# Performance work log

Hardware: AMD Instinct MI355X
Metric: run time of the kernel (lower is better)

## Reference

```python
import jax, jax.numpy as jnp
import numpy as np

B, S, D = 4, 1024, 1024
H, DK, DV = 16, 64, 32
SCALE = float(np.sqrt(DK))


def setup_inputs() -> dict:
    key = jax.random.key(0)
    ks = jax.random.split(key, 10)
    std = 0.02
    x = jax.random.normal(ks[0], (B, S, D), dtype=jnp.float32)
    # Per-head projection weights stacked: y = x @ W + b (equiv to torch Linear)
    Wq = jax.random.normal(ks[1], (H, D, DK), dtype=jnp.float32) * std
    bq = jax.random.normal(ks[2], (H, DK), dtype=jnp.float32) * std
    Wk = jax.random.normal(ks[3], (H, D, DK), dtype=jnp.float32) * std
    bk = jax.random.normal(ks[4], (H, DK), dtype=jnp.float32) * std
    Wv = jax.random.normal(ks[5], (H, D, DV), dtype=jnp.float32) * std
    bv = jax.random.normal(ks[6], (H, DV), dtype=jnp.float32) * std
    Wo = jax.random.normal(ks[7], (H * DV, D), dtype=jnp.float32) * std
    bo = jax.random.normal(ks[8], (D,), dtype=jnp.float32) * std
    return {"x": x, "Wq": Wq, "bq": bq, "Wk": Wk, "bk": bk,
            "Wv": Wv, "bv": bv, "Wo": Wo, "bo": bo}


def reference(x, Wq, bq, Wk, bk, Wv, bv, Wo, bo):
    # batched per-head projections (vectorizes the torch per-head loop)
    q = jnp.einsum('bsd,hdk->bhsk', x, Wq) + bq[None, :, None, :]
    k = jnp.einsum('bsd,hdk->bhsk', x, Wk) + bk[None, :, None, :]
    v = jnp.einsum('bsd,hdv->bhsv', x, Wv) + bv[None, :, None, :]
    # scaled dot-product attention (no mask path)
    scores = jnp.einsum('bhsk,bhtk->bhst', q, k) / SCALE  # [B,H,S,S]
    weights = jax.nn.softmax(scores, axis=-1)
    out_h = jnp.einsum('bhst,bhtv->bhsv', weights, v)      # [B,H,S,DV]
    # concat heads in head order (matches torch.cat over head_outputs)
    concat = out_h.transpose(0, 2, 1, 3).reshape(B, S, H * DV)
    output = concat @ Wo + bo  # dropout p=0 / eval -> identity
    return (output, weights)
```

## Files before the change

### kernel.cpp

```cpp
#include <hip/hip_runtime.h>
#include <cstdint>
#include <cstddef>

#define BB 4
#define SS 1024
#define DD 1024
#define HH 16
#define DKK 64
#define DVV 32
#define LOG2E 1.44269504088896340736f

typedef __bf16 bf16_t;
typedef __bf16 bf16x8 __attribute__((ext_vector_type(8)));
typedef float f32x4 __attribute__((ext_vector_type(4)));

__device__ inline bf16x8 cvt8(const float* __restrict__ s) {
  float4 a = *(const float4*)s;
  float4 b = *(const float4*)(s + 4);
  bf16x8 r;
  r[0] = (__bf16)a.x; r[1] = (__bf16)a.y; r[2] = (__bf16)a.z; r[3] = (__bf16)a.w;
  r[4] = (__bf16)b.x; r[5] = (__bf16)b.y; r[6] = (__bf16)b.z; r[7] = (__bf16)b.w;
  return r;
}

__global__ __launch_bounds__(256) void transpose_cvt_kernel(
    const float* __restrict__ src, bf16_t* __restrict__ dst,
    int M, int N, size_t srcStride, size_t dstStride) {
  __shared__ __align__(16) bf16_t T[64][72];
  const int tid = threadIdx.x;
  const int n0 = blockIdx.x * 64, m0 = blockIdx.y * 64;
  const float* s = src + (size_t)blockIdx.z * srcStride;
  bf16_t* d = dst + (size_t)blockIdx.z * dstStride;
  const int rr = tid >> 3, c8 = (tid & 7) * 8;

  if (n0 + c8 < N) {
#pragma unroll
    for (int mm = rr; mm < 64; mm += 32) {
      const float* p = s + (size_t)(m0 + mm) * N + n0 + c8;
      float4 a = *(const float4*)p;
      float4 b = *(const float4*)(p + 4);
      T[c8 + 0][mm] = (__bf16)a.x; T[c8 + 1][mm] = (__bf16)a.y;
      T[c8 + 2][mm] = (__bf16)a.z; T[c8 + 3][mm] = (__bf16)a.w;
      T[c8 + 4][mm] = (__bf16)b.x; T[c8 + 5][mm] = (__bf16)b.y;
      T[c8 + 6][mm] = (__bf16)b.z; T[c8 + 7][mm] = (__bf16)b.w;
    }
  }
  __syncthreads();
#pragma unroll
  for (int rn = rr; rn < 64; rn += 32) {
    if (n0 + rn < N)
      *(uint4*)(d + (size_t)(n0 + rn) * M + m0 + c8) = *(uint4*)&T[rn][c8];
  }
}

__global__ __launch_bounds__(256) void qkv_gemm_kernel(
    const float* __restrict__ X, const bf16_t* __restrict__ WT,
    const float* __restrict__ bq, const float* __restrict__ bk,
    const float* __restrict__ bv,
    bf16_t* __restrict__ Qw, bf16_t* __restrict__ Kw, bf16_t* __restrict__ VT) {
  __shared__ __align__(16) bf16_t As[64][72];
  __shared__ __align__(16) bf16_t Bs[64][72];
  const int m0 = blockIdx.x * 64;
  const int n0 = blockIdx.y * 64;
  const int tid = threadIdx.x;
  const int wave = tid >> 6;
  const int lane = tid & 63;
  const int g = lane >> 4;
  const int ln = lane & 15;
  const int r = tid >> 3;
  const int c8 = (tid & 7) * 8;

  f32x4 acc[4] = {};

  for (int k0 = 0; k0 < 1024; k0 += 64) {
    *(bf16x8*)&As[r][c8]      = cvt8(X + (size_t)(m0 + r) * 1024 + k0 + c8);
    *(bf16x8*)&As[r + 32][c8] = cvt8(X + (size_t)(m0 + r + 32) * 1024 + k0 + c8);
    *(uint4*)&Bs[r][c8]      = *(const uint4*)(WT + (size_t)(n0 + r) * 1024 + k0 + c8);
    *(uint4*)&Bs[r + 32][c8] = *(const uint4*)(WT + (size_t)(n0 + r + 32) * 1024 + k0 + c8);
    __syncthreads();
#pragma unroll
    for (int ks = 0; ks < 2; ks++) {
      bf16x8 a = *(const bf16x8*)&As[wave * 16 + ln][ks * 32 + g * 8];
#pragma unroll
      for (int ns = 0; ns < 4; ns++) {
        bf16x8 b = *(const bf16x8*)&Bs[ns * 16 + ln][ks * 32 + g * 8];
        acc[ns] = __builtin_amdgcn_mfma_f32_16x16x32_bf16(a, b, acc[ns], 0, 0, 0);
      }
    }
    __syncthreads();
  }

#pragma unroll
  for (int ns = 0; ns < 4; ns++) {
    int c = n0 + ns * 16 + ln;
    float bias = (c < 1024) ? bq[c] : (c < 2048 ? bk[c - 1024] : bv[c - 2048]);
#pragma unroll
    for (int i = 0; i < 4; i++) {
      int m = m0 + wave * 16 + g * 4 + i;
      float v = acc[ns][i] + bias;
      int b_ = m >> 10, s_ = m & 1023;
      if (c < 1024) {
        int h = c >> 6, k = c & 63;
        Qw[(((size_t)(b_ * HH + h)) * SS + s_) * DKK + k] = (__bf16)(v * 0.125f);
      } else if (c < 2048) {
        int c2 = c - 1024;
        int h = c2 >> 6, k = c2 & 63;
        Kw[(((size_t)(b_ * HH + h)) * SS + s_) * DKK + k] = (__bf16)v;
      } else {
        int c2 = c - 2048;
        int h = c2 >> 5, vv = c2 & 31;
        VT[(((size_t)(b_ * HH + h)) * DVV + vv) * SS + s_] = (__bf16)v;
      }
    }
  }
}

__global__ __launch_bounds__(256) void attn_softmax_kernel(
    const bf16_t* __restrict__ Qw, const bf16_t* __restrict__ Kw,
    float* __restrict__ Wout) {
  __shared__ __align__(16) bf16_t Qs[64][72];
  __shared__ __align__(16) bf16_t Ks[64][72];
  const int bh = blockIdx.y;
  const int m0 = blockIdx.x * 64;
  const int tid = threadIdx.x;
  const int wave = tid >> 6;
  const int lane = tid & 63;
  const int g = lane >> 4;
  const int ln = lane & 15;
  const int r = tid >> 3;
  const int c8 = (tid & 7) * 8;

  const bf16_t* Qbase = Qw + (size_t)bh * SS * DKK;
  const bf16_t* Kbase = Kw + (size_t)bh * SS * DKK;

  *(uint4*)&Qs[r][c8]      = *(const uint4*)(Qbase + (size_t)(m0 + r) * DKK + c8);
  *(uint4*)&Qs[r + 32][c8] = *(const uint4*)(Qbase + (size_t)(m0 + r + 32) * DKK + c8);
  __syncthreads();

  float mrun[4] = {-1e30f, -1e30f, -1e30f, -1e30f};
  float lrun[4] = {0.f, 0.f, 0.f, 0.f};

  for (int jt = 0; jt < 16; jt++) {
    *(uint4*)&Ks[r][c8]      = *(const uint4*)(Kbase + (size_t)(jt * 64 + r) * DKK + c8);
    *(uint4*)&Ks[r + 32][c8] = *(const uint4*)(Kbase + (size_t)(jt * 64 + r + 32) * DKK + c8);
    __syncthreads();
    f32x4 acc[4] = {};
#pragma unroll
    for (int ks = 0; ks < 2; ks++) {
      bf16x8 a = *(const bf16x8*)&Qs[wave * 16 + ln][ks * 32 + g * 8];
#pragma unroll
      for (int ns = 0; ns < 4; ns++) {
        bf16x8 b = *(const bf16x8*)&Ks[ns * 16 + ln][ks * 32 + g * 8];
        acc[ns] = __builtin_amdgcn_mfma_f32_16x16x32_bf16(a, b, acc[ns], 0, 0, 0);
      }
    }
#pragma unroll
    for (int ns = 0; ns < 4; ns++) {
#pragma unroll
      for (int i = 0; i < 4; i++) {
        float p = acc[ns][i] * LOG2E;
        float mo = mrun[i];
        float mn = fmaxf(mo, p);
        lrun[i] = lrun[i] * exp2f(mo - mn) + exp2f(p - mn);
        mrun[i] = mn;
      }
    }
    __syncthreads();
  }

#pragma unroll
  for (int i = 0; i < 4; i++) {
    float m = mrun[i], l = lrun[i];
#pragma unroll
    for (int d = 1; d < 16; d <<= 1) {
      float om = __shfl_xor(m, d);
      float ol = __shfl_xor(l, d);
      float nm = fmaxf(m, om);
      l = l * exp2f(m - nm) + ol * exp2f(om - nm);
      m = nm;
    }
    mrun[i] = m;
    lrun[i] = 1.0f / l;
  }

  float* wbase = Wout + (size_t)bh * SS * SS;
  for (int jt = 0; jt < 16; jt++) {
    *(uint4*)&Ks[r][c8]      = *(const uint4*)(Kbase + (size_t)(jt * 64 + r) * DKK + c8);
    *(uint4*)&Ks[r + 32][c8] = *(const uint4*)(Kbase + (size_t)(jt * 64 + r + 32) * DKK + c8);
    __syncthreads();
    f32x4 acc[4] = {};
#pragma unroll
    for (int ks = 0; ks < 2; ks++) {
      bf16x8 a = *(const bf16x8*)&Qs[wave * 16 + ln][ks * 32 + g * 8];
#pragma unroll
      for (int ns = 0; ns < 4; ns++) {
        bf16x8 b = *(const bf16x8*)&Ks[ns * 16 + ln][ks * 32 + g * 8];
        acc[ns] = __builtin_amdgcn_mfma_f32_16x16x32_bf16(a, b, acc[ns], 0, 0, 0);
      }
    }
#pragma unroll
    for (int ns = 0; ns < 4; ns++) {
      int col = jt * 64 + ns * 16 + ln;
#pragma unroll
      for (int i = 0; i < 4; i++) {
        int row = m0 + wave * 16 + g * 4 + i;
        wbase[(size_t)row * SS + col] =
            exp2f(acc[ns][i] * LOG2E - mrun[i]) * lrun[i];
      }
    }
    __syncthreads();
  }
}

__global__ __launch_bounds__(256) void av_gemm_kernel(
    const float* __restrict__ Wts, const bf16_t* __restrict__ VT,
    bf16_t* __restrict__ concat) {
  __shared__ __align__(16) bf16_t As[64][72];
  __shared__ __align__(16) bf16_t Bs[32][72];
  const int bh = blockIdx.y;
  const int b_ = bh >> 4, h = bh & 15;
  const int m0 = blockIdx.x * 64;
  const int tid = threadIdx.x;
  const int wave = tid >> 6;
  const int lane = tid & 63;
  const int g = lane >> 4;
  const int ln = lane & 15;
  const int r = tid >> 3;
  const int c8 = (tid & 7) * 8;

  const float* wbase = Wts + (size_t)bh * SS * SS;
  const bf16_t* vbase = VT + (size_t)bh * DVV * SS;

  f32x4 acc[2] = {};

  for (int k0 = 0; k0 < 1024; k0 += 64) {
    *(bf16x8*)&As[r][c8]      = cvt8(wbase + (size_t)(m0 + r) * SS + k0 + c8);
    *(bf16x8*)&As[r + 32][c8] = cvt8(wbase + (size_t)(m0 + r + 32) * SS + k0 + c8);
    *(uint4*)&Bs[r][c8]       = *(const uint4*)(vbase + (size_t)r * SS + k0 + c8);
    __syncthreads();
#pragma unroll
    for (int ks = 0; ks < 2; ks++) {
      bf16x8 a = *(const bf16x8*)&As[wave * 16 + ln][ks * 32 + g * 8];
#pragma unroll
      for (int ns = 0; ns < 2; ns++) {
        bf16x8 b = *(const bf16x8*)&Bs[ns * 16 + ln][ks * 32 + g * 8];
        acc[ns] = __builtin_amdgcn_mfma_f32_16x16x32_bf16(a, b, acc[ns], 0, 0, 0);
      }
    }
    __syncthreads();
  }

#pragma unroll
  for (int ns = 0; ns < 2; ns++) {
    int col = ns * 16 + ln;
#pragma unroll
    for (int i = 0; i < 4; i++) {
      int s_ = m0 + wave * 16 + g * 4 + i;
      concat[((size_t)(b_ * SS + s_)) * (HH * DVV) + h * DVV + col] =
          (__bf16)acc[ns][i];
    }
  }
}

__global__ __launch_bounds__(256) void out_gemm_kernel(
    const bf16_t* __restrict__ Cc, const bf16_t* __restrict__ WoT,
    const float* __restrict__ bo, float* __restrict__ Out) {
  __shared__ __align__(16) bf16_t As[64][72];
  __shared__ __align__(16) bf16_t Bs[64][72];
  const int m0 = blockIdx.x * 64;
  const int n0 = blockIdx.y * 64;
  const int tid = threadIdx.x;
  const int wave = tid >> 6;
  const int lane = tid & 63;
  const int g = lane >> 4;
  const int ln = lane & 15;
  const int r = tid >> 3;
  const int c8 = (tid & 7) * 8;

  f32x4 acc[4] = {};

  for (int k0 = 0; k0 < 512; k0 += 64) {
    *(uint4*)&As[r][c8]      = *(const uint4*)(Cc  + (size_t)(m0 + r) * 512 + k0 + c8);
    *(uint4*)&As[r + 32][c8] = *(const uint4*)(Cc  + (size_t)(m0 + r + 32) * 512 + k0 + c8);
    *(uint4*)&Bs[r][c8]      = *(const uint4*)(WoT + (size_t)(n0 + r) * 512 + k0 + c8);
    *(uint4*)&Bs[r + 32][c8] = *(const uint4*)(WoT + (size_t)(n0 + r + 32) * 512 + k0 + c8);
    __syncthreads();
#pragma unroll
    for (int ks = 0; ks < 2; ks++) {
      bf16x8 a = *(const bf16x8*)&As[wave * 16 + ln][ks * 32 + g * 8];
#pragma unroll
      for (int ns = 0; ns < 4; ns++) {
        bf16x8 b = *(const bf16x8*)&Bs[ns * 16 + ln][ks * 32 + g * 8];
        acc[ns] = __builtin_amdgcn_mfma_f32_16x16x32_bf16(a, b, acc[ns], 0, 0, 0);
      }
    }
    __syncthreads();
  }

#pragma unroll
  for (int ns = 0; ns < 4; ns++) {
    int col = n0 + ns * 16 + ln;
    float bias = bo[col];
#pragma unroll
    for (int i = 0; i < 4; i++) {
      int m = m0 + wave * 16 + g * 4 + i;
      Out[(size_t)m * DD + col] = acc[ns][i] + bias;
    }
  }
}

extern "C" void kernel_launch(void* const* d_in, const int* in_sizes, int n_in,
                              void* d_out, int out_size, void* d_ws, size_t ws_size,
                              hipStream_t stream) {
  const float* x  = (const float*)d_in[0];
  const float* Wq = (const float*)d_in[1];
  const float* bq = (const float*)d_in[2];
  const float* Wk = (const float*)d_in[3];
  const float* bk = (const float*)d_in[4];
  const float* Wv = (const float*)d_in[5];
  const float* bv = (const float*)d_in[6];
  const float* Wo = (const float*)d_in[7];
  const float* bo = (const float*)d_in[8];

  float* out = (float*)d_out;
  float* weights_out = out + (size_t)BB * SS * DD;

  char* ws = (char*)d_ws;
  bf16_t* WcatT = (bf16_t*)ws;  ws += (size_t)2560 * 1024 * 2;
  bf16_t* WoT   = (bf16_t*)ws;  ws += (size_t)1024 * 512 * 2;
  bf16_t* Qw    = (bf16_t*)ws;  ws += (size_t)BB * HH * SS * DKK * 2;
  bf16_t* Kw    = (bf16_t*)ws;  ws += (size_t)BB * HH * SS * DKK * 2;
  bf16_t* VT    = (bf16_t*)ws;  ws += (size_t)BB * HH * DVV * SS * 2;
  bf16_t* concat = (bf16_t*)ws;

  transpose_cvt_kernel<<<dim3(1, 16, 16), 256, 0, stream>>>(
      Wq, WcatT,                     1024, 64, (size_t)1024 * 64, (size_t)64 * 1024);
  transpose_cvt_kernel<<<dim3(1, 16, 16), 256, 0, stream>>>(
      Wk, WcatT + (size_t)1024 * 1024, 1024, 64, (size_t)1024 * 64, (size_t)64 * 1024);
  transpose_cvt_kernel<<<dim3(1, 16, 16), 256, 0, stream>>>(
      Wv, WcatT + (size_t)2048 * 1024, 1024, 32, (size_t)1024 * 32, (size_t)32 * 1024);
  transpose_cvt_kernel<<<dim3(16, 8, 1), 256, 0, stream>>>(
      Wo, WoT, 512, 1024, 0, 0);

  qkv_gemm_kernel<<<dim3(64, 40), 256, 0, stream>>>(
      x, WcatT, bq, bk, bv, Qw, Kw, VT);
  attn_softmax_kernel<<<dim3(16, 64), 256, 0, stream>>>(Qw, Kw, weights_out);
  av_gemm_kernel<<<dim3(16, 64), 256, 0, stream>>>(weights_out, VT, concat);
  out_gemm_kernel<<<dim3(64, 16), 256, 0, stream>>>(concat, WoT, bo, out);
}
```

Before: 500.9 us.

## Fuse softmax-weights and attention-value GEMM into one kernel

Merges the softmax kernel and the attention-times-V GEMM into a single kernel. In the second pass over key tiles it writes the normalized probabilities to the fp32 weights output, keeps a bf16 copy in shared memory, and multiplies it by the V tile right away. This removes the separate kernel's re-read of the large fp32 weights tensor from global memory, along with its fp32-to-bf16 conversion. In exchange it adds extra shared-memory buffers, and a per-tile V load and MFMA work inside the second pass.

```diff
diff --git a/kernel.cpp b/kernel.cpp
--- a/kernel.cpp
+++ b/kernel.cpp
@@ -115,108 +115,14 @@
   }
 }
 
-__global__ __launch_bounds__(256) void attn_softmax_kernel(
+__global__ __launch_bounds__(256) void attn_fused_kernel(
     const bf16_t* __restrict__ Qw, const bf16_t* __restrict__ Kw,
-    float* __restrict__ Wout) {
+    const bf16_t* __restrict__ VT, float* __restrict__ Wout,
+    bf16_t* __restrict__ concat) {
   __shared__ __align__(16) bf16_t Qs[64][72];
   __shared__ __align__(16) bf16_t Ks[64][72];
-  const int bh = blockIdx.y;
-  const int m0 = blockIdx.x * 64;
-  const int tid = threadIdx.x;
-  const int wave = tid >> 6;
-  const int lane = tid & 63;
-  const int g = lane >> 4;
-  const int ln = lane & 15;
-  const int r = tid >> 3;
-  const int c8 = (tid & 7) * 8;
-
-  const bf16_t* Qbase = Qw + (size_t)bh * SS * DKK;
-  const bf16_t* Kbase = Kw + (size_t)bh * SS * DKK;
-
-  *(uint4*)&Qs[r][c8]      = *(const uint4*)(Qbase + (size_t)(m0 + r) * DKK + c8);
-  *(uint4*)&Qs[r + 32][c8] = *(const uint4*)(Qbase + (size_t)(m0 + r + 32) * DKK + c8);
-  __syncthreads();
-
-  float mrun[4] = {-1e30f, -1e30f, -1e30f, -1e30f};
-  float lrun[4] = {0.f, 0.f, 0.f, 0.f};
-
-  for (int jt = 0; jt < 16; jt++) {
-    *(uint4*)&Ks[r][c8]      = *(const uint4*)(Kbase + (size_t)(jt * 64 + r) * DKK + c8);
-    *(uint4*)&Ks[r + 32][c8] = *(const uint4*)(Kbase + (size_t)(jt * 64 + r + 32) * DKK + c8);
-    __syncthreads();
-    f32x4 acc[4] = {};
-#pragma unroll
-    for (int ks = 0; ks < 2; ks++) {
-      bf16x8 a = *(const bf16x8*)&Qs[wave * 16 + ln][ks * 32 + g * 8];
-#pragma unroll
-      for (int ns = 0; ns < 4; ns++) {
-        bf16x8 b = *(const bf16x8*)&Ks[ns * 16 + ln][ks * 32 + g * 8];
-        acc[ns] = __builtin_amdgcn_mfma_f32_16x16x32_bf16(a, b, acc[ns], 0, 0, 0);
-      }
-    }
-#pragma unroll
-    for (int ns = 0; ns < 4; ns++) {
-#pragma unroll
-      for (int i = 0; i < 4; i++) {
-        float p = acc[ns][i] * LOG2E;
-        float mo = mrun[i];
-        float mn = fmaxf(mo, p);
-        lrun[i] = lrun[i] * exp2f(mo - mn) + exp2f(p - mn);
-        mrun[i] = mn;
-      }
-    }
-    __syncthreads();
-  }
-
-#pragma unroll
-  for (int i = 0; i < 4; i++) {
-    float m = mrun[i], l = lrun[i];
-#pragma unroll
-    for (int d = 1; d < 16; d <<= 1) {
-      float om = __shfl_xor(m, d);
-      float ol = __shfl_xor(l, d);
-      float nm = fmaxf(m, om);
-      l = l * exp2f(m - nm) + ol * exp2f(om - nm);
-      m = nm;
-    }
-    mrun[i] = m;
-    lrun[i] = 1.0f / l;
-  }
-
-  float* wbase = Wout + (size_t)bh * SS * SS;
-  for (int jt = 0; jt < 16; jt++) {
-    *(uint4*)&Ks[r][c8]      = *(const uint4*)(Kbase + (size_t)(jt * 64 + r) * DKK + c8);
-    *(uint4*)&Ks[r + 32][c8] = *(const uint4*)(Kbase + (size_t)(jt * 64 + r + 32) * DKK + c8);
-    __syncthreads();
-    f32x4 acc[4] = {};
-#pragma unroll
-    for (int ks = 0; ks < 2; ks++) {
-      bf16x8 a = *(const bf16x8*)&Qs[wave * 16 + ln][ks * 32 + g * 8];
-#pragma unroll
-      for (int ns = 0; ns < 4; ns++) {
-        bf16x8 b = *(const bf16x8*)&Ks[ns * 16 + ln][ks * 32 + g * 8];
-        acc[ns] = __builtin_amdgcn_mfma_f32_16x16x32_bf16(a, b, acc[ns], 0, 0, 0);
-      }
-    }
-#pragma unroll
-    for (int ns = 0; ns < 4; ns++) {
-      int col = jt * 64 + ns * 16 + ln;
-#pragma unroll
-      for (int i = 0; i < 4; i++) {
-        int row = m0 + wave * 16 + g * 4 + i;
-        wbase[(size_t)row * SS + col] =
-            exp2f(acc[ns][i] * LOG2E - mrun[i]) * lrun[i];
-      }
-    }
-    __syncthreads();
-  }
-}
-
-__global__ __launch_bounds__(256) void av_gemm_kernel(
-    const float* __restrict__ Wts, const bf16_t* __restrict__ VT,
-    bf16_t* __restrict__ concat) {
-  __shared__ __align__(16) bf16_t As[64][72];
-  __shared__ __align__(16) bf16_t Bs[32][72];
+  __shared__ __align__(16) bf16_t Ps[64][72];
+  __shared__ __align__(16) bf16_t Vs[32][72];
   const int bh = blockIdx.y;
   const int b_ = bh >> 4, h = bh & 15;
   const int m0 = blockIdx.x * 64;
@@ -228,36 +134,108 @@
   const int r = tid >> 3;
   const int c8 = (tid & 7) * 8;
 
-  const float* wbase = Wts + (size_t)bh * SS * SS;
+  const bf16_t* Qbase = Qw + (size_t)bh * SS * DKK;
+  const bf16_t* Kbase = Kw + (size_t)bh * SS * DKK;
   const bf16_t* vbase = VT + (size_t)bh * DVV * SS;
 
-  f32x4 acc[2] = {};
-
-  for (int k0 = 0; k0 < 1024; k0 += 64) {
-    *(bf16x8*)&As[r][c8]      = cvt8(wbase + (size_t)(m0 + r) * SS + k0 + c8);
-    *(bf16x8*)&As[r + 32][c8] = cvt8(wbase + (size_t)(m0 + r + 32) * SS + k0 + c8);
-    *(uint4*)&Bs[r][c8]       = *(const uint4*)(vbase + (size_t)r * SS + k0 + c8);
-    __syncthreads();
-#pragma unroll
-    for (int ks = 0; ks < 2; ks++) {
-      bf16x8 a = *(const bf16x8*)&As[wave * 16 + ln][ks * 32 + g * 8];
-#pragma unroll
-      for (int ns = 0; ns < 2; ns++) {
-        bf16x8 b = *(const bf16x8*)&Bs[ns * 16 + ln][ks * 32 + g * 8];
+  *(uint4*)&Qs[r][c8]      = *(const uint4*)(Qbase + (size_t)(m0 + r) * DKK + c8);
+  *(uint4*)&Qs[r + 32][c8] = *(const uint4*)(Qbase + (size_t)(m0 + r + 32) * DKK + c8);
+
+  float mrun[4] = {-1e30f, -1e30f, -1e30f, -1e30f};
+  float lrun[4] = {0.f, 0.f, 0.f, 0.f};
+
+  for (int jt = 0; jt < 16; jt++) {
+    __syncthreads();
+    *(uint4*)&Ks[r][c8]      = *(const uint4*)(Kbase + (size_t)(jt * 64 + r) * DKK + c8);
+    *(uint4*)&Ks[r + 32][c8] = *(const uint4*)(Kbase + (size_t)(jt * 64 + r + 32) * DKK + c8);
+    __syncthreads();
+    f32x4 acc[4] = {};
+#pragma unroll
+    for (int ks = 0; ks < 2; ks++) {
+      bf16x8 a = *(const bf16x8*)&Qs[wave * 16 + ln][ks * 32 + g * 8];
+#pragma unroll
+      for (int ns = 0; ns < 4; ns++) {
+        bf16x8 b = *(const bf16x8*)&Ks[ns * 16 + ln][ks * 32 + g * 8];
         acc[ns] = __builtin_amdgcn_mfma_f32_16x16x32_bf16(a, b, acc[ns], 0, 0, 0);
       }
     }
-    __syncthreads();
-  }
-
-#pragma unroll
-  for (int ns = 0; ns < 2; ns++) {
-    int col = ns * 16 + ln;
+#pragma unroll
+    for (int ns = 0; ns < 4; ns++) {
+#pragma unroll
+      for (int i = 0; i < 4; i++) {
+        float p = acc[ns][i] * LOG2E;
+        float mo = mrun[i];
+        float mn = fmaxf(mo, p);
+        lrun[i] = lrun[i] * exp2f(mo - mn) + exp2f(p - mn);
+        mrun[i] = mn;
+      }
+    }
+  }
+
+#pragma unroll
+  for (int i = 0; i < 4; i++) {
+    float m = mrun[i], l = lrun[i];
+#pragma unroll
+    for (int d = 1; d < 16; d <<= 1) {
+      float om = __shfl_xor(m, d);
+      float ol = __shfl_xor(l, d);
+      float nm = fmaxf(m, om);
+      l = l * exp2f(m - nm) + ol * exp2f(om - nm);
+      m = nm;
+    }
+    mrun[i] = m;
+    lrun[i] = 1.0f / l;
+  }
+
+  float* wbase = Wout + (size_t)bh * SS * SS;
+  f32x4 acc_o[2] = {};
+  for (int jt = 0; jt < 16; jt++) {
+    __syncthreads();
+    *(uint4*)&Ks[r][c8]      = *(const uint4*)(Kbase + (size_t)(jt * 64 + r) * DKK + c8);
+    *(uint4*)&Ks[r + 32][c8] = *(const uint4*)(Kbase + (size_t)(jt * 64 + r + 32) * DKK + c8);
+    *(uint4*)&Vs[tid >> 3][c8] =
+        *(const uint4*)(vbase + (size_t)(tid >> 3) * SS + jt * 64 + c8);
+    __syncthreads();
+    f32x4 acc[4] = {};
+#pragma unroll
+    for (int ks = 0; ks < 2; ks++) {
+      bf16x8 a = *(const bf16x8*)&Qs[wave * 16 + ln][ks * 32 + g * 8];
+#pragma unroll
+      for (int ns = 0; ns < 4; ns++) {
+        bf16x8 b = *(const bf16x8*)&Ks[ns * 16 + ln][ks * 32 + g * 8];
+        acc[ns] = __builtin_amdgcn_mfma_f32_16x16x32_bf16(a, b, acc[ns], 0, 0, 0);
+      }
+    }
+#pragma unroll
+    for (int ns = 0; ns < 4; ns++) {
+      int col = jt * 64 + ns * 16 + ln;
+#pragma unroll
+      for (int i = 0; i < 4; i++) {
+        int mr = wave * 16 + g * 4 + i;
+        float w = exp2f(acc[ns][i] * LOG2E - mrun[i]) * lrun[i];
+        wbase[(size_t)(m0 + mr) * SS + col] = w;
+        Ps[mr][ns * 16 + ln] = (__bf16)w;
+      }
+    }
+#pragma unroll
+    for (int ks = 0; ks < 2; ks++) {
+      bf16x8 a = *(const bf16x8*)&Ps[wave * 16 + ln][ks * 32 + g * 8];
+#pragma unroll
+      for (int n2 = 0; n2 < 2; n2++) {
+        bf16x8 b = *(const bf16x8*)&Vs[n2 * 16 + ln][ks * 32 + g * 8];
+        acc_o[n2] = __builtin_amdgcn_mfma_f32_16x16x32_bf16(a, b, acc_o[n2], 0, 0, 0);
+      }
+    }
+  }
+
+#pragma unroll
+  for (int n2 = 0; n2 < 2; n2++) {
+    int col = n2 * 16 + ln;
 #pragma unroll
     for (int i = 0; i < 4; i++) {
       int s_ = m0 + wave * 16 + g * 4 + i;
       concat[((size_t)(b_ * SS + s_)) * (HH * DVV) + h * DVV + col] =
-          (__bf16)acc[ns][i];
+          (__bf16)acc_o[n2][i];
     }
   }
 }
@@ -344,7 +322,7 @@
 
   qkv_gemm_kernel<<<dim3(64, 40), 256, 0, stream>>>(
       x, WcatT, bq, bk, bv, Qw, Kw, VT);
-  attn_softmax_kernel<<<dim3(16, 64), 256, 0, stream>>>(Qw, Kw, weights_out);
-  av_gemm_kernel<<<dim3(16, 64), 256, 0, stream>>>(weights_out, VT, concat);
+  attn_fused_kernel<<<dim3(16, 64), 256, 0, stream>>>(
+      Qw, Kw, VT, weights_out, concat);
   out_gemm_kernel<<<dim3(64, 16), 256, 0, stream>>>(concat, WoT, bo, out);
 }
```

Result: faster. 455.2 us (-9.1%).
